# Kernel optimization log

Hardware: AMD Instinct MI355X
Metric: run time of the kernel (lower is better)

## Reference

```python
import jax, jax.numpy as jnp
import numpy as np

N_NODES = 100000
K_HOPS = 10
ALPHA = 0.1


def gcn_conv(x, src, dst, W, b, num_nodes):
    # GCNConv: linear first (cheaper: out_dim small), then D^-1/2 (A+I) D^-1/2 aggregation
    h = x @ W  # [N, out]
    deg = jax.ops.segment_sum(jnp.ones_like(dst, dtype=h.dtype), dst, num_segments=num_nodes)
    dinv = jnp.where(deg > 0, jax.lax.rsqrt(deg), 0.0)
    norm = dinv[src] * dinv[dst]  # [E]
    msg = h[src] * norm[:, None]
    out = jax.ops.segment_sum(msg, dst, num_segments=num_nodes)
    return out + b


def _with_self_loops(edge_index, num_nodes):
    loops = jnp.arange(num_nodes, dtype=edge_index.dtype)
    src = jnp.concatenate([edge_index[0], loops])
    dst = jnp.concatenate([edge_index[1], loops])
    return src, dst


def setup_inputs() -> dict:
    key = jax.random.key(0)
    ks = jax.random.split(key, 8)
    n_feat, hidden, n_cls, n_edges = 512, 16, 7, 3200000
    x = jax.random.normal(ks[0], (N_NODES, n_feat), dtype=jnp.float32)
    edge_index = jax.random.randint(ks[1], (2, n_edges), 0, N_NODES, dtype=jnp.int64)
    W1 = jax.random.normal(ks[2], (n_feat, hidden), dtype=jnp.float32) * 0.05
    b1 = jnp.zeros((hidden,), dtype=jnp.float32)
    Wl = jax.random.normal(ks[3], (hidden, hidden), dtype=jnp.float32) * 0.25
    bl = jnp.zeros((hidden,), dtype=jnp.float32)
    W2 = jax.random.normal(ks[4], (hidden, n_cls), dtype=jnp.float32) * 0.25
    b2 = jnp.zeros((n_cls,), dtype=jnp.float32)
    return {"x": x, "edge_index": edge_index, "W1": W1, "b1": b1, "Wl": Wl, "bl": bl, "W2": W2, "b2": b2}


def reference(x, edge_index, W1, b1, Wl, bl, W2, b2):
    src, dst = _with_self_loops(edge_index, N_NODES)
    h = jax.nn.relu(gcn_conv(x, src, dst, W1, b1, N_NODES))
    def body(h, _):
        h = ALPHA * jax.nn.relu(h @ Wl + bl) + (1.0 - ALPHA) * h
        return h, None
    h, _ = jax.lax.scan(body, h, None, length=K_HOPS)
    out = gcn_conv(h, src, dst, W2, b2, N_NODES)
    return jax.nn.log_softmax(out, axis=1)
```

## Files before the change

kernel.cpp:

```cpp
#include <hip/hip_runtime.h>
#include <math.h>

#define N_NODES 100000
#define N_EDGES 3200000
#define F_IN    512
#define HID     16
#define NCLS    7
#define ALPHA   0.1f
#define K_HOPS  10

#define SHIFT   7
#define BWIDTH  128
#define NBUCK   ((N_NODES + BWIDTH - 1) / BWIDTH)
#define CHUNK   8192
#define EPT     (CHUNK / 256)
#define A3_BLOCKS ((N_EDGES + CHUNK - 1) / CHUNK)

#define OFF_BCNT    0u
#define OFF_BSTART  1024u
#define OFF_BCUR    2048u
#define OFF_RP      3072u
#define OFF_DINV    103424u
#define OFF_COL     203776u
#define OFF_BINNED  3403776u
#define OFF_H0      6603776u
#define OFF_H1      8203776u
#define OFF_Z       9803776u

__global__ void k_bhist(const int* __restrict__ dst, int* __restrict__ bcnt) {
    __shared__ int h[NBUCK];
    int tid = threadIdx.x;
    for (int i = tid; i < NBUCK; i += 256) h[i] = 0;
    __syncthreads();
    for (int e = blockIdx.x * 256 + tid; e < N_EDGES; e += gridDim.x * 256)
        atomicAdd(&h[dst[e] >> SHIFT], 1);
    __syncthreads();
    for (int i = tid; i < NBUCK; i += 256) {
        int v = h[i];
        if (v) atomicAdd(&bcnt[i], v);
    }
}

__global__ void k_bscan(const int* __restrict__ bcnt, int* __restrict__ bstart,
                        int* __restrict__ bcur) {
    __shared__ int s[1024];
    int tid = threadIdx.x;
    int v = (tid < NBUCK) ? bcnt[tid] : 0;
    s[tid] = v;
    __syncthreads();
    for (int off = 1; off < 1024; off <<= 1) {
        int t = (tid >= off) ? s[tid - off] : 0;
        __syncthreads();
        s[tid] += t;
        __syncthreads();
    }
    if (tid < NBUCK) {
        int ex = s[tid] - v;
        bstart[tid] = ex;
        bcur[tid] = ex;
    }
    if (tid == 0) bstart[NBUCK] = N_EDGES;
}

__global__ void k_bin(const int* __restrict__ src, const int* __restrict__ dst,
                      int* __restrict__ bcur, unsigned int* __restrict__ binned) {
    __shared__ int ha[NBUCK];
    __shared__ int gbase[NBUCK];
    __shared__ int lcur[NBUCK];
    int tid = threadIdx.x;
    int e0 = blockIdx.x * CHUNK;
    int e1 = e0 + CHUNK;
    if (e1 > N_EDGES) e1 = N_EDGES;
    for (int i = tid; i < NBUCK; i += 256) ha[i] = 0;
    __syncthreads();
    int dloc[EPT];
#pragma unroll
    for (int i = 0; i < EPT; i++) {
        int e = e0 + tid + i * 256;
        dloc[i] = (e < e1) ? dst[e] : -1;
        if (dloc[i] >= 0) atomicAdd(&ha[dloc[i] >> SHIFT], 1);
    }
    __syncthreads();
    for (int s = tid; s < NBUCK; s += 256) {
        int c = ha[s];
        lcur[s] = 0;
        gbase[s] = c ? atomicAdd(&bcur[s], c) : 0;
    }
    __syncthreads();
#pragma unroll
    for (int i = 0; i < EPT; i++) {
        int d = dloc[i];
        if (d >= 0) {
            int e = e0 + tid + i * 256;
            int bk = d >> SHIFT;
            int idx = atomicAdd(&lcur[bk], 1);
            binned[gbase[bk] + idx] =
                ((unsigned int)(d & (BWIDTH - 1)) << 17) | (unsigned int)src[e];
        }
    }
}

__global__ void k_csr(const unsigned int* __restrict__ binned, const int* __restrict__ bstart,
                      int* __restrict__ rp, float* __restrict__ dinv, int* __restrict__ col) {
    __shared__ int cnt[BWIDTH];
    __shared__ int s[BWIDTH];
    __shared__ int cur[BWIDTH];
    int tid = threadIdx.x;
    int b = blockIdx.x;
    int base = b << SHIFT;
    int e0 = bstart[b], e1 = bstart[b + 1];
    if (tid < BWIDTH) cnt[tid] = 0;
    __syncthreads();
    for (int e = e0 + tid; e < e1; e += 256)
        atomicAdd(&cnt[binned[e] >> 17], 1);
    __syncthreads();
    int v = 0;
    if (tid < BWIDTH) { v = cnt[tid]; s[tid] = v; }
    __syncthreads();
    for (int off = 1; off < BWIDTH; off <<= 1) {
        int t = 0;
        if (tid < BWIDTH && tid >= off) t = s[tid - off];
        __syncthreads();
        if (tid < BWIDTH) s[tid] += t;
        __syncthreads();
    }
    if (tid < BWIDTH) {
        int ex = s[tid] - v;
        cur[tid] = ex;
        int node = base + tid;
        if (node < N_NODES) {
            rp[node] = e0 + ex;
            dinv[node] = rsqrtf((float)(v + 1));
        }
    }
    if (b == 0 && tid == 0) rp[N_NODES] = N_EDGES;
    __syncthreads();
    for (int e = e0 + tid; e < e1; e += 256) {
        unsigned int w = binned[e];
        int ln = (int)(w >> 17);
        int p = atomicAdd(&cur[ln], 1);
        col[e0 + p] = (int)(w & 0x1FFFFu);
    }
}

#define XW_ROWS 64
#define XW_KT   32
#define XW_S    65
#define XW_NT   (F_IN / XW_KT)
__global__ void k_xw1(const float* __restrict__ x, const float* __restrict__ W,
                      const float* __restrict__ dinv, float* __restrict__ h0s) {
    __shared__ float xT[2][XW_KT * XW_S];
    int tid = threadIdx.x;
    int rowBase = blockIdx.x * XW_ROWS;

    int rf0 = tid >> 3, kq = tid & 7;
    int rf1 = rf0 + 32;
    bool v0 = (rowBase + rf0) < N_NODES;
    bool v1 = (rowBase + rf1) < N_NODES;
    const float* xrow0 = x + (size_t)(rowBase + rf0) * F_IN;
    const float* xrow1 = x + (size_t)(rowBase + rf1) * F_IN;

    int r  = tid & 63;
    int cg = __builtin_amdgcn_readfirstlane(tid >> 6);
    const float4* W4 = (const float4*)W;

    float4 zero4 = make_float4(0.f, 0.f, 0.f, 0.f);
    float4 acc = zero4;
    float4 ld0 = v0 ? ((const float4*)xrow0)[kq] : zero4;
    float4 ld1 = v1 ? ((const float4*)xrow1)[kq] : zero4;

    for (int kt = 0; kt < XW_NT; kt++) {
        int buf = kt & 1;
        float* xb = xT[buf];
        int kb = kq * 4;
        xb[(kb + 0) * XW_S + rf0] = ld0.x;
        xb[(kb + 1) * XW_S + rf0] = ld0.y;
        xb[(kb + 2) * XW_S + rf0] = ld0.z;
        xb[(kb + 3) * XW_S + rf0] = ld0.w;
        xb[(kb + 0) * XW_S + rf1] = ld1.x;
        xb[(kb + 1) * XW_S + rf1] = ld1.y;
        xb[(kb + 2) * XW_S + rf1] = ld1.z;
        xb[(kb + 3) * XW_S + rf1] = ld1.w;
        if (kt + 1 < XW_NT) {
            const float4* p0 = (const float4*)(xrow0 + (kt + 1) * XW_KT);
            const float4* p1 = (const float4*)(xrow1 + (kt + 1) * XW_KT);
            ld0 = v0 ? p0[kq] : zero4;
            ld1 = v1 ? p1[kq] : zero4;
        }
        __syncthreads();
        const float* xr = &xb[r];
#pragma unroll
        for (int k = 0; k < XW_KT; k++) {
            float xv = xr[k * XW_S];
            float4 w4 = W4[(kt * XW_KT + k) * 4 + cg];
            acc.x += xv * w4.x;
            acc.y += xv * w4.y;
            acc.z += xv * w4.z;
            acc.w += xv * w4.w;
        }
    }
    int node = rowBase + r;
    if (node < N_NODES) {
        float dv = dinv[node];
        float4 o;
        o.x = dv * acc.x; o.y = dv * acc.y; o.z = dv * acc.z; o.w = dv * acc.w;
        ((float4*)h0s)[(size_t)node * 4 + cg] = o;
    }
}

__global__ void k_agg1(const float* __restrict__ h0s, const int* __restrict__ rp,
                       const int* __restrict__ col, const float* __restrict__ dinv,
                       const float* __restrict__ b1, float* __restrict__ h1) {
    int node = (blockIdx.x * blockDim.x + threadIdx.x) >> 6;
    if (node >= N_NODES) return;
    int lane = threadIdx.x & 63;
    int c = lane & 15, eo = lane >> 4;
    int e0 = rp[node], e1 = rp[node + 1];
    float acc = 0.f;
    for (int e = e0 + eo; e < e1; e += 4)
        acc += h0s[(size_t)col[e] * HID + c];
    acc += __shfl_xor(acc, 16);
    acc += __shfl_xor(acc, 32);
    float o = dinv[node] * (acc + h0s[(size_t)node * HID + c]) + b1[c];
    if (eo == 0) h1[(size_t)node * HID + c] = fmaxf(o, 0.f);
}

__global__ void k_hops(const float* __restrict__ h1, const float* __restrict__ Wl,
                       const float* __restrict__ bl, const float* __restrict__ W2,
                       const float* __restrict__ dinv, float* __restrict__ zs) {
    int node = blockIdx.x * blockDim.x + threadIdx.x;
    if (node >= N_NODES) return;
    float h[HID];
    const float4* h4 = (const float4*)(h1 + (size_t)node * HID);
#pragma unroll
    for (int q = 0; q < HID / 4; q++) {
        float4 v = h4[q];
        h[q * 4 + 0] = v.x; h[q * 4 + 1] = v.y;
        h[q * 4 + 2] = v.z; h[q * 4 + 3] = v.w;
    }
    for (int it = 0; it < K_HOPS; it++) {
        float tm[HID];
#pragma unroll
        for (int c = 0; c < HID; c++) tm[c] = bl[c];
#pragma unroll
        for (int k = 0; k < HID; k++) {
            float hk = h[k];
#pragma unroll
            for (int c = 0; c < HID; c++) tm[c] += hk * Wl[k * HID + c];
        }
#pragma unroll
        for (int c = 0; c < HID; c++)
            h[c] = ALPHA * fmaxf(tm[c], 0.f) + (1.f - ALPHA) * h[c];
    }
    float dv = dinv[node];
    float zz[8];
#pragma unroll
    for (int c = 0; c < 8; c++) zz[c] = 0.f;
#pragma unroll
    for (int k = 0; k < HID; k++) {
        float hk = h[k];
#pragma unroll
        for (int c = 0; c < NCLS; c++) zz[c] += hk * W2[k * NCLS + c];
    }
    float4* z4 = (float4*)(zs + (size_t)node * 8);
    float4 v0, v1;
    v0.x = dv * zz[0]; v0.y = dv * zz[1]; v0.z = dv * zz[2]; v0.w = dv * zz[3];
    v1.x = dv * zz[4]; v1.y = dv * zz[5]; v1.z = dv * zz[6]; v1.w = 0.f;
    z4[0] = v0; z4[1] = v1;
}

__global__ void k_agg2(const float* __restrict__ zs, const int* __restrict__ rp,
                       const int* __restrict__ col, const float* __restrict__ dinv,
                       const float* __restrict__ b2, float* __restrict__ out) {
    int node = (blockIdx.x * blockDim.x + threadIdx.x) >> 6;
    if (node >= N_NODES) return;
    int lane = threadIdx.x & 63;
    int c = lane & 7, eo = lane >> 3;
    int e0 = rp[node], e1 = rp[node + 1];
    float acc = 0.f;
    for (int e = e0 + eo; e < e1; e += 8)
        acc += zs[(size_t)col[e] * 8 + c];
    acc += __shfl_xor(acc, 8);
    acc += __shfl_xor(acc, 16);
    acc += __shfl_xor(acc, 32);
    float o = dinv[node] * (acc + zs[(size_t)node * 8 + c]) + ((c < NCLS) ? b2[c] : 0.f);
    float val = (c < NCLS) ? o : -INFINITY;
    float m = val;
    m = fmaxf(m, __shfl_xor(m, 1));
    m = fmaxf(m, __shfl_xor(m, 2));
    m = fmaxf(m, __shfl_xor(m, 4));
    float ex = (c < NCLS) ? expf(o - m) : 0.f;
    float ss = ex;
    ss += __shfl_xor(ss, 1);
    ss += __shfl_xor(ss, 2);
    ss += __shfl_xor(ss, 4);
    if (eo == 0 && c < NCLS) out[(size_t)node * NCLS + c] = o - m - logf(ss);
}

extern "C" void kernel_launch(void* const* d_in, const int* in_sizes, int n_in,
                              void* d_out, int out_size, void* d_ws, size_t ws_size,
                              hipStream_t stream) {
    const float* x  = (const float*)d_in[0];
    const int*   ei = (const int*)d_in[1];
    const float* W1 = (const float*)d_in[2];
    const float* b1 = (const float*)d_in[3];
    const float* Wl = (const float*)d_in[4];
    const float* bl = (const float*)d_in[5];
    const float* W2 = (const float*)d_in[6];
    const float* b2 = (const float*)d_in[7];
    float* out = (float*)d_out;

    int*   wsI = (int*)d_ws;
    float* wsF = (float*)d_ws;
    int*          bcnt   = wsI + OFF_BCNT;
    int*          bstart = wsI + OFF_BSTART;
    int*          bcur   = wsI + OFF_BCUR;
    int*          rp     = wsI + OFF_RP;
    float*        dinv   = wsF + OFF_DINV;
    int*          col    = wsI + OFF_COL;
    unsigned int* binned = (unsigned int*)(wsI + OFF_BINNED);
    float*        h0s    = wsF + OFF_H0;
    float*        h1     = wsF + OFF_H1;
    float*        zs     = wsF + OFF_Z;

    const int* src = ei;
    const int* dst = ei + N_EDGES;

    hipMemsetAsync(bcnt, 0, NBUCK * sizeof(int), stream);

    k_bhist<<<1024, 256, 0, stream>>>(dst, bcnt);
    k_bscan<<<1, 1024, 0, stream>>>(bcnt, bstart, bcur);
    k_bin<<<A3_BLOCKS, 256, 0, stream>>>(src, dst, bcur, binned);
    k_csr<<<NBUCK, 256, 0, stream>>>(binned, bstart, rp, dinv, col);
    k_xw1<<<(N_NODES + XW_ROWS - 1) / XW_ROWS, 256, 0, stream>>>(x, W1, dinv, h0s);
    k_agg1<<<(N_NODES * 64 + 255) / 256, 256, 0, stream>>>(h0s, rp, col, dinv, b1, h1);
    k_hops<<<(N_NODES + 255) / 256, 256, 0, stream>>>(h1, Wl, bl, W2, dinv, zs);
    k_agg2<<<(N_NODES * 64 + 255) / 256, 256, 0, stream>>>(zs, rp, col, dinv, b2, out);
}
```

Baseline: 597.7 us.

## Aggregate directly from bucketed edges with shared-memory atomics, dropping CSR build

Removes the per-bucket CSR construction (scan and column scatter) and keeps only a degree count to compute dinv. Both aggregation kernels now run one block per 128-node bucket, read the binned (local dst, src) words directly and accumulate into padded shared-memory tiles with atomics. This removes the col/rp writes and reads and one full pass over the edges. In exchange it adds LDS atomic contention and leaves only 782 blocks for each aggregation kernel.

```diff
diff --git a/kernel.cpp b/kernel.cpp
--- a/kernel.cpp
+++ b/kernel.cpp
@@ -19,9 +19,7 @@
 #define OFF_BCNT    0u
 #define OFF_BSTART  1024u
 #define OFF_BCUR    2048u
-#define OFF_RP      3072u
 #define OFF_DINV    103424u
-#define OFF_COL     203776u
 #define OFF_BINNED  3403776u
 #define OFF_H0      6603776u
 #define OFF_H1      8203776u
@@ -100,47 +98,20 @@
     }
 }
 
-__global__ void k_csr(const unsigned int* __restrict__ binned, const int* __restrict__ bstart,
-                      int* __restrict__ rp, float* __restrict__ dinv, int* __restrict__ col) {
+__global__ void k_dinv(const unsigned int* __restrict__ binned, const int* __restrict__ bstart,
+                       float* __restrict__ dinv) {
     __shared__ int cnt[BWIDTH];
-    __shared__ int s[BWIDTH];
-    __shared__ int cur[BWIDTH];
     int tid = threadIdx.x;
     int b = blockIdx.x;
-    int base = b << SHIFT;
     int e0 = bstart[b], e1 = bstart[b + 1];
     if (tid < BWIDTH) cnt[tid] = 0;
     __syncthreads();
     for (int e = e0 + tid; e < e1; e += 256)
         atomicAdd(&cnt[binned[e] >> 17], 1);
     __syncthreads();
-    int v = 0;
-    if (tid < BWIDTH) { v = cnt[tid]; s[tid] = v; }
-    __syncthreads();
-    for (int off = 1; off < BWIDTH; off <<= 1) {
-        int t = 0;
-        if (tid < BWIDTH && tid >= off) t = s[tid - off];
-        __syncthreads();
-        if (tid < BWIDTH) s[tid] += t;
-        __syncthreads();
-    }
-    if (tid < BWIDTH) {
-        int ex = s[tid] - v;
-        cur[tid] = ex;
-        int node = base + tid;
-        if (node < N_NODES) {
-            rp[node] = e0 + ex;
-            dinv[node] = rsqrtf((float)(v + 1));
-        }
-    }
-    if (b == 0 && tid == 0) rp[N_NODES] = N_EDGES;
-    __syncthreads();
-    for (int e = e0 + tid; e < e1; e += 256) {
-        unsigned int w = binned[e];
-        int ln = (int)(w >> 17);
-        int p = atomicAdd(&cur[ln], 1);
-        col[e0 + p] = (int)(w & 0x1FFFFu);
-    }
+    int node = (b << SHIFT) + tid;
+    if (tid < BWIDTH && node < N_NODES)
+        dinv[node] = rsqrtf((float)(cnt[tid] + 1));
 }
 
 #define XW_ROWS 64
@@ -208,21 +179,36 @@
     }
 }
 
-__global__ void k_agg1(const float* __restrict__ h0s, const int* __restrict__ rp,
-                       const int* __restrict__ col, const float* __restrict__ dinv,
+#define AGG1_T 512
+#define A1_S   17
+__global__ void k_agg1(const float* __restrict__ h0s, const unsigned int* __restrict__ binned,
+                       const int* __restrict__ bstart, const float* __restrict__ dinv,
                        const float* __restrict__ b1, float* __restrict__ h1) {
-    int node = (blockIdx.x * blockDim.x + threadIdx.x) >> 6;
-    if (node >= N_NODES) return;
-    int lane = threadIdx.x & 63;
-    int c = lane & 15, eo = lane >> 4;
-    int e0 = rp[node], e1 = rp[node + 1];
-    float acc = 0.f;
-    for (int e = e0 + eo; e < e1; e += 4)
-        acc += h0s[(size_t)col[e] * HID + c];
-    acc += __shfl_xor(acc, 16);
-    acc += __shfl_xor(acc, 32);
-    float o = dinv[node] * (acc + h0s[(size_t)node * HID + c]) + b1[c];
-    if (eo == 0) h1[(size_t)node * HID + c] = fmaxf(o, 0.f);
+    __shared__ float acc[BWIDTH * A1_S];
+    int tid = threadIdx.x;
+    int b = blockIdx.x;
+    int base = b << SHIFT;
+    int e0 = bstart[b], e1 = bstart[b + 1];
+    for (int i = tid; i < BWIDTH * A1_S; i += AGG1_T) acc[i] = 0.f;
+    __syncthreads();
+    int c = tid & 15;
+    int eo = tid >> 4;
+    for (int e = e0 + eo; e < e1; e += AGG1_T / 16) {
+        unsigned int w = binned[e];
+        int srcn = (int)(w & 0x1FFFFu);
+        int ln = (int)(w >> 17);
+        float v = h0s[(size_t)srcn * HID + c];
+        atomicAdd(&acc[ln * A1_S + c], v);
+    }
+    __syncthreads();
+    for (int i = tid; i < BWIDTH * HID; i += AGG1_T) {
+        int ln = i >> 4, cc = i & 15;
+        int node = base + ln;
+        if (node < N_NODES) {
+            float o = dinv[node] * (acc[ln * A1_S + cc] + h0s[(size_t)node * HID + cc]) + b1[cc];
+            h1[(size_t)node * HID + cc] = fmaxf(o, 0.f);
+        }
+    }
 }
 
 __global__ void k_hops(const float* __restrict__ h1, const float* __restrict__ Wl,
@@ -269,32 +255,44 @@
     z4[0] = v0; z4[1] = v1;
 }
 
-__global__ void k_agg2(const float* __restrict__ zs, const int* __restrict__ rp,
-                       const int* __restrict__ col, const float* __restrict__ dinv,
+#define A2_S 9
+__global__ void k_agg2(const float* __restrict__ zs, const unsigned int* __restrict__ binned,
+                       const int* __restrict__ bstart, const float* __restrict__ dinv,
                        const float* __restrict__ b2, float* __restrict__ out) {
-    int node = (blockIdx.x * blockDim.x + threadIdx.x) >> 6;
-    if (node >= N_NODES) return;
-    int lane = threadIdx.x & 63;
-    int c = lane & 7, eo = lane >> 3;
-    int e0 = rp[node], e1 = rp[node + 1];
-    float acc = 0.f;
-    for (int e = e0 + eo; e < e1; e += 8)
-        acc += zs[(size_t)col[e] * 8 + c];
-    acc += __shfl_xor(acc, 8);
-    acc += __shfl_xor(acc, 16);
-    acc += __shfl_xor(acc, 32);
-    float o = dinv[node] * (acc + zs[(size_t)node * 8 + c]) + ((c < NCLS) ? b2[c] : 0.f);
-    float val = (c < NCLS) ? o : -INFINITY;
-    float m = val;
-    m = fmaxf(m, __shfl_xor(m, 1));
-    m = fmaxf(m, __shfl_xor(m, 2));
-    m = fmaxf(m, __shfl_xor(m, 4));
-    float ex = (c < NCLS) ? expf(o - m) : 0.f;
-    float ss = ex;
-    ss += __shfl_xor(ss, 1);
-    ss += __shfl_xor(ss, 2);
-    ss += __shfl_xor(ss, 4);
-    if (eo == 0 && c < NCLS) out[(size_t)node * NCLS + c] = o - m - logf(ss);
+    __shared__ float acc[BWIDTH * A2_S];
+    int tid = threadIdx.x;
+    int b = blockIdx.x;
+    int base = b << SHIFT;
+    int e0 = bstart[b], e1 = bstart[b + 1];
+    for (int i = tid; i < BWIDTH * A2_S; i += 512) acc[i] = 0.f;
+    __syncthreads();
+    int c = tid & 7;
+    int eo = tid >> 3;
+    for (int e = e0 + eo; e < e1; e += 64) {
+        unsigned int w = binned[e];
+        int srcn = (int)(w & 0x1FFFFu);
+        int ln = (int)(w >> 17);
+        atomicAdd(&acc[ln * A2_S + c], zs[(size_t)srcn * 8 + c]);
+    }
+    __syncthreads();
+    int g = tid >> 3;
+    for (int ln = g; ln < BWIDTH; ln += 64) {
+        int node = base + ln;
+        if (node >= N_NODES) continue;
+        float o = dinv[node] * (acc[ln * A2_S + c] + zs[(size_t)node * 8 + c])
+                  + ((c < NCLS) ? b2[c] : 0.f);
+        float val = (c < NCLS) ? o : -INFINITY;
+        float m = val;
+        m = fmaxf(m, __shfl_xor(m, 1));
+        m = fmaxf(m, __shfl_xor(m, 2));
+        m = fmaxf(m, __shfl_xor(m, 4));
+        float ex = (c < NCLS) ? expf(o - m) : 0.f;
+        float ss = ex;
+        ss += __shfl_xor(ss, 1);
+        ss += __shfl_xor(ss, 2);
+        ss += __shfl_xor(ss, 4);
+        if (c < NCLS) out[(size_t)node * NCLS + c] = o - m - logf(ss);
+    }
 }
 
 extern "C" void kernel_launch(void* const* d_in, const int* in_sizes, int n_in,
@@ -315,9 +313,7 @@
     int*          bcnt   = wsI + OFF_BCNT;
     int*          bstart = wsI + OFF_BSTART;
     int*          bcur   = wsI + OFF_BCUR;
-    int*          rp     = wsI + OFF_RP;
     float*        dinv   = wsF + OFF_DINV;
-    int*          col    = wsI + OFF_COL;
     unsigned int* binned = (unsigned int*)(wsI + OFF_BINNED);
     float*        h0s    = wsF + OFF_H0;
     float*        h1     = wsF + OFF_H1;
@@ -331,9 +327,9 @@
     k_bhist<<<1024, 256, 0, stream>>>(dst, bcnt);
     k_bscan<<<1, 1024, 0, stream>>>(bcnt, bstart, bcur);
     k_bin<<<A3_BLOCKS, 256, 0, stream>>>(src, dst, bcur, binned);
-    k_csr<<<NBUCK, 256, 0, stream>>>(binned, bstart, rp, dinv, col);
+    k_dinv<<<NBUCK, 256, 0, stream>>>(binned, bstart, dinv);
     k_xw1<<<(N_NODES + XW_ROWS - 1) / XW_ROWS, 256, 0, stream>>>(x, W1, dinv, h0s);
-    k_agg1<<<(N_NODES * 64 + 255) / 256, 256, 0, stream>>>(h0s, rp, col, dinv, b1, h1);
+    k_agg1<<<NBUCK, AGG1_T, 0, stream>>>(h0s, binned, bstart, dinv, b1, h1);
     k_hops<<<(N_NODES + 255) / 256, 256, 0, stream>>>(h1, Wl, bl, W2, dinv, zs);
-    k_agg2<<<(N_NODES * 64 + 255) / 256, 256, 0, stream>>>(zs, rp, col, dinv, b2, out);
-}
+    k_agg2<<<NBUCK, 512, 0, stream>>>(zs, binned, bstart, dinv, b2, out);
+}
```

Result: slower. 953.4 us (+59.5%).
